# Performance work log

Hardware: AMD Instinct MI355X
Metric: run time of the kernel (lower is better)

## Reference

```python
import math
import jax, jax.numpy as jnp
import numpy as np

B, N, M, C, H, POS = 2, 2048, 64, 256, 8, 6
D = C // H  # head_dim = 32
SCALE = 1.0 / math.sqrt(D)
LAMDA = 1.0


def setup_inputs() -> dict:
    key = jax.random.key(0)
    ks = jax.random.split(key, 15)
    s = 0.05
    return {
        "pairwise_g": jax.random.normal(ks[0], (B, N, N, POS), jnp.float32),
        "coset_functions": jax.random.normal(ks[1], (B, N, C), jnp.float32),
        "mask": jnp.ones((B, N), dtype=bool),
        "Wq": jax.random.normal(ks[2], (C, C), jnp.float32) * s,
        "bq": jax.random.normal(ks[3], (C,), jnp.float32) * s,
        "Wk": jax.random.normal(ks[4], (C, C), jnp.float32) * s,
        "bk": jax.random.normal(ks[5], (C,), jnp.float32) * s,
        "Wl": jax.random.normal(ks[6], (C, POS), jnp.float32) * s,
        "bl": jax.random.normal(ks[7], (C,), jnp.float32) * s,
        "u": jax.random.normal(ks[8], (H, D), jnp.float32) * s,
        "v": jax.random.normal(ks[9], (H, D), jnp.float32) * s,
        "Wi": jax.random.normal(ks[10], (C, C), jnp.float32) * s,
        "bi": jax.random.normal(ks[11], (C,), jnp.float32) * s,
        "Wo": jax.random.normal(ks[12], (C, C), jnp.float32) * s,
        "bo": jax.random.normal(ks[13], (C,), jnp.float32) * s,
    }


def reference(pairwise_g, coset_functions, mask, Wq, bq, Wk, bk, Wl, bl, u, v, Wi, bi, Wo, bo):
    # ---- extract_neighbourhoods (mc_samples=M, fill=1.0 -> k == k_ball, permutation irrelevant)
    dists = jnp.linalg.norm(pairwise_g, axis=-1)                      # (B,N,N)
    dists = jnp.where(mask[:, None, :], dists, jnp.float32(1e8))
    _, nbhd_idx = jax.lax.top_k(-dists, M)                            # (B,N,M) nearest neighbors
    nbhd_pg = jnp.take_along_axis(pairwise_g, nbhd_idx[..., None], axis=2)  # (B,N,M,POS)
    gather_rows = jax.vmap(lambda arr, ix: arr[ix])                   # gather along point axis per batch
    nbhd_cf = gather_rows(coset_functions, nbhd_idx)                  # (B,N,M,C)
    nbhd_mask = gather_rows(mask, nbhd_idx)                           # (B,N,M)

    # ---- RelativePositionKernel
    Q = (coset_functions @ Wq.T + bq).reshape(B, N, H, D).transpose(0, 2, 1, 3)  # (B,H,N,D)
    K = (coset_functions @ Wk.T + bk).reshape(B, N, H, D).transpose(0, 2, 1, 3)  # (B,H,N,D)
    e = (nbhd_pg @ Wl.T + bl).reshape(B, N, M, H, D)                  # (B,N,M,H,D)

    S = jnp.einsum('bhnd,bhkd->bhnk', Q, K)                           # dense scores (as original)
    Sg = jnp.take_along_axis(S, nbhd_idx[:, None, :, :], axis=3)      # (B,H,N,M)
    e_term = jnp.einsum('bnmhd,bhnd->bhnm', e, Q + v[None, :, None, :])
    uK = jnp.einsum('hd,bhkd->bhk', u, K)                             # (B,H,N)
    uKg = jnp.take_along_axis(uK[:, :, None, :], nbhd_idx[:, None, :, :], axis=3)  # (B,H,N,M)
    A = (Sg + LAMDA * e_term + uKg) * SCALE
    A = A.transpose(0, 2, 3, 1)                                       # (B,N,M,H)

    # ---- masked softmax over neighbors
    A = jnp.where(nbhd_mask[..., None], A, jnp.float32(-1e38))
    attn = jax.nn.softmax(A, axis=2)                                  # (B,N,M,H)

    # ---- value projection + weighted sum + output linear
    Vv = (nbhd_cf @ Wi.T + bi).reshape(B, N, M, H, D)                 # (B,N,M,H,D)
    out = jnp.einsum('bnmh,bnmhd->bnhd', attn, Vv).reshape(B, N, C)
    out = out @ Wo.T + bo                                             # (B,N,c_out)
    return out
```

## Files before the change

### kernel.cpp

```cpp
#include <hip/hip_runtime.h>
#include <stdint.h>

#define NB 2
#define NN 2048
#define MM 64
#define CC 256
#define HH 8
#define DD 32
#define PP 6
#define ATT_SCALE 0.17677669529663687f

typedef __attribute__((ext_vector_type(8))) short short8;
typedef __attribute__((ext_vector_type(4))) float f32x4;

__device__ __forceinline__ uint16_t f2bf(float f) {
  union { float f; uint32_t u; } c; c.f = f;
  return (uint16_t)((c.u + 0x7fffu + ((c.u >> 16) & 1u)) >> 16);
}
__device__ __forceinline__ float blo(uint32_t u) {
  union { uint32_t u; float f; } c; c.u = u << 16; return c.f;
}
__device__ __forceinline__ float bhi(uint32_t u) {
  union { uint32_t u; float f; } c; c.u = u & 0xffff0000u; return c.f;
}
__device__ __forceinline__ short8 pack8(float4 a, float4 b) {
  short8 r;
  r[0] = (short)f2bf(a.x); r[1] = (short)f2bf(a.y);
  r[2] = (short)f2bf(a.z); r[3] = (short)f2bf(a.w);
  r[4] = (short)f2bf(b.x); r[5] = (short)f2bf(b.y);
  r[6] = (short)f2bf(b.z); r[7] = (short)f2bf(b.w);
  return r;
}

__global__ __launch_bounds__(64) void k_gemm_qkv(
    const float* __restrict__ A,
    const float* __restrict__ W0, const float* __restrict__ W1, const float* __restrict__ W2,
    const float* __restrict__ b0, const float* __restrict__ b1, const float* __restrict__ b2,
    float* __restrict__ Qo, uint16_t* __restrict__ Ko, uint16_t* __restrict__ Vo) {
  const int z = blockIdx.z;
  const float* W = (z == 0) ? W0 : ((z == 1) ? W1 : W2);
  const float* bias = (z == 0) ? b0 : ((z == 1) ? b1 : b2);

  const int lane = threadIdx.x;
  const int m = lane & 15;
  const int quad = lane >> 4;
  const int row0 = blockIdx.x * 16;
  const int c0 = blockIdx.y * 64;

  f32x4 acc0 = {0.f, 0.f, 0.f, 0.f};
  f32x4 acc1 = {0.f, 0.f, 0.f, 0.f};
  f32x4 acc2 = {0.f, 0.f, 0.f, 0.f};
  f32x4 acc3 = {0.f, 0.f, 0.f, 0.f};

#pragma unroll
  for (int k0 = 0; k0 < CC; k0 += 32) {
    const float4* ap = (const float4*)(A + (size_t)(row0 + m) * CC + k0 + quad * 8);
    const float4* bp0 = (const float4*)(W + (size_t)(c0 + 0 + m) * CC + k0 + quad * 8);
    const float4* bp1 = (const float4*)(W + (size_t)(c0 + 16 + m) * CC + k0 + quad * 8);
    const float4* bp2 = (const float4*)(W + (size_t)(c0 + 32 + m) * CC + k0 + quad * 8);
    const float4* bp3 = (const float4*)(W + (size_t)(c0 + 48 + m) * CC + k0 + quad * 8);
    const short8 a = pack8(ap[0], ap[1]);
    const short8 f0 = pack8(bp0[0], bp0[1]);
    const short8 f1 = pack8(bp1[0], bp1[1]);
    const short8 f2 = pack8(bp2[0], bp2[1]);
    const short8 f3 = pack8(bp3[0], bp3[1]);
    acc0 = __builtin_amdgcn_mfma_f32_16x16x32_bf16(a, f0, acc0, 0, 0, 0);
    acc1 = __builtin_amdgcn_mfma_f32_16x16x32_bf16(a, f1, acc1, 0, 0, 0);
    acc2 = __builtin_amdgcn_mfma_f32_16x16x32_bf16(a, f2, acc2, 0, 0, 0);
    acc3 = __builtin_amdgcn_mfma_f32_16x16x32_bf16(a, f3, acc3, 0, 0, 0);
  }

  const int orow = row0 + quad * 4;
  f32x4 accs[4] = {acc0, acc1, acc2, acc3};
#pragma unroll
  for (int f = 0; f < 4; ++f) {
    const int col = c0 + f * 16 + m;
    const float bv = bias[col];
#pragma unroll
    for (int r = 0; r < 4; ++r) {
      const float val = accs[f][r] + bv;
      const size_t o = (size_t)(orow + r) * CC + col;
      if (z == 0) Qo[o] = val;
      else if (z == 1) Ko[o] = f2bf(val);
      else Vo[o] = f2bf(val);
    }
  }
}

__global__ __launch_bounds__(64) void k_gemm_out(const uint16_t* __restrict__ A,
                                                 const float* __restrict__ W,
                                                 const float* __restrict__ bias,
                                                 float* __restrict__ O) {
  const int lane = threadIdx.x;
  const int m = lane & 15;
  const int quad = lane >> 4;
  const int row0 = blockIdx.x * 16;
  const int c0 = blockIdx.y * 32;

  f32x4 acc0 = {0.f, 0.f, 0.f, 0.f};
  f32x4 acc1 = {0.f, 0.f, 0.f, 0.f};

#pragma unroll
  for (int k0 = 0; k0 < CC; k0 += 32) {
    const short8 a = *(const short8*)(A + (size_t)(row0 + m) * CC + k0 + quad * 8);
    const float4* bp0 = (const float4*)(W + (size_t)(c0 + 0 + m) * CC + k0 + quad * 8);
    const float4* bp1 = (const float4*)(W + (size_t)(c0 + 16 + m) * CC + k0 + quad * 8);
    const short8 f0 = pack8(bp0[0], bp0[1]);
    const short8 f1 = pack8(bp1[0], bp1[1]);
    acc0 = __builtin_amdgcn_mfma_f32_16x16x32_bf16(a, f0, acc0, 0, 0, 0);
    acc1 = __builtin_amdgcn_mfma_f32_16x16x32_bf16(a, f1, acc1, 0, 0, 0);
  }

  const int orow = row0 + quad * 4;
  f32x4 accs[2] = {acc0, acc1};
#pragma unroll
  for (int f = 0; f < 2; ++f) {
    const int col = c0 + f * 16 + m;
    const float bv = bias[col];
#pragma unroll
    for (int r = 0; r < 4; ++r) {
      O[(size_t)(orow + r) * CC + col] = accs[f][r] + bv;
    }
  }
}

__global__ __launch_bounds__(256) void k_fused(const float* __restrict__ pg,
                                               const float* __restrict__ Q,
                                               const uint16_t* __restrict__ K,
                                               const uint16_t* __restrict__ V,
                                               const float* __restrict__ Wl,
                                               const float* __restrict__ bl,
                                               const float* __restrict__ u,
                                               const float* __restrict__ v,
                                               uint16_t* __restrict__ attnV) {
  const int row = blockIdx.x;
  const int b = row >> 11;
  const int t = threadIdx.x;
  const int wave = t >> 6;
  const int lane = t & 63;

  __shared__ float s_mn[4], s_mx[4];
  __shared__ uint32_t s_wsum[4];
  __shared__ uint32_t s_hist[256];
  __shared__ uint32_t s_scan[256];
  __shared__ float s_cd[NN];
  __shared__ int   s_cj[NN];
  __shared__ int s_tbin;
  __shared__ uint32_t s_c0;
  __shared__ int s_cw;
  __shared__ int s_ct;
  __shared__ int s_idx[MM];
  __shared__ float s_npg[MM][7];
  __shared__ float s_qu[CC];
  __shared__ float s_wt[HH][8];
  __shared__ float s_sc[HH][MM];
  __shared__ float s_part[CC];

  const float qv_ = Q[(size_t)row * CC + t];
  s_qu[t] = qv_ + u[t];
  if (t < MM) s_idx[t] = t;

  const float4* base = (const float4*)(pg + (size_t)row * NN * PP);

  float d[8];
  float mn = 3.4e38f, mx = -3.4e38f;
#pragma unroll
  for (int i = 0; i < 4; i++) {
    const int j0 = i * 512 + 2 * t;
    const float4 qa = base[(size_t)(j0 >> 1) * 3 + 0];
    const float4 qb = base[(size_t)(j0 >> 1) * 3 + 1];
    const float4 qc = base[(size_t)(j0 >> 1) * 3 + 2];
    float s0 = __fmul_rn(qa.x, qa.x);
    s0 = __fadd_rn(s0, __fmul_rn(qa.y, qa.y));
    s0 = __fadd_rn(s0, __fmul_rn(qa.z, qa.z));
    s0 = __fadd_rn(s0, __fmul_rn(qa.w, qa.w));
    s0 = __fadd_rn(s0, __fmul_rn(qb.x, qb.x));
    s0 = __fadd_rn(s0, __fmul_rn(qb.y, qb.y));
    float s1 = __fmul_rn(qb.z, qb.z);
    s1 = __fadd_rn(s1, __fmul_rn(qb.w, qb.w));
    s1 = __fadd_rn(s1, __fmul_rn(qc.x, qc.x));
    s1 = __fadd_rn(s1, __fmul_rn(qc.y, qc.y));
    s1 = __fadd_rn(s1, __fmul_rn(qc.z, qc.z));
    s1 = __fadd_rn(s1, __fmul_rn(qc.w, qc.w));
    const float d0 = __fsqrt_rn(s0);
    const float d1 = __fsqrt_rn(s1);
    d[2 * i] = d0; d[2 * i + 1] = d1;
    mn = fminf(mn, fminf(d0, d1));
    mx = fmaxf(mx, fmaxf(d0, d1));
  }

#pragma unroll
  for (int off = 32; off; off >>= 1) {
    mn = fminf(mn, __shfl_xor(mn, off));
    mx = fmaxf(mx, __shfl_xor(mx, off));
  }
  if (lane == 0) { s_mn[wave] = mn; s_mx[wave] = mx; }
  s_hist[t] = 0;
  __syncthreads();
  mn = fminf(fminf(s_mn[0], s_mn[1]), fminf(s_mn[2], s_mn[3]));
  mx = fmaxf(fmaxf(s_mx[0], s_mx[1]), fmaxf(s_mx[2], s_mx[3]));
  const float range = mx - mn;
  const float scale = (range > 0.f) ? (256.0f / range) : 0.f;

  int bins[8];
#pragma unroll
  for (int i = 0; i < 8; i++) {
    int bn = (int)((d[i] - mn) * scale);
    bn = (bn > 255) ? 255 : (bn < 0 ? 0 : bn);
    bins[i] = bn;
    atomicAdd(&s_hist[bn], 1u);
  }
  __syncthreads();

  {
    uint32_t x = s_hist[t];
#pragma unroll
    for (int off = 1; off < 64; off <<= 1) {
      const uint32_t y = __shfl_up(x, off);
      if (lane >= off) x += y;
    }
    if (lane == 63) s_wsum[wave] = x;
    __syncthreads();
    uint32_t pre = 0;
    for (int w = 0; w < wave; w++) pre += s_wsum[w];
    x += pre;
    s_scan[t] = x;
  }
  if (t == 0) { s_cw = 0; s_ct = 0; }
  __syncthreads();

  if (s_scan[t] >= (uint32_t)MM && (t == 0 || s_scan[t - 1] < (uint32_t)MM)) {
    s_tbin = t;
    s_c0 = (t == 0) ? 0u : s_scan[t - 1];
  }
  __syncthreads();

  const int tbin = s_tbin;
  const int c0 = (int)s_c0;

#pragma unroll
  for (int i = 0; i < 8; i++) {
    const int j = (i >> 1) * 512 + 2 * t + (i & 1);
    if (bins[i] < tbin) {
      const int pos = atomicAdd(&s_cw, 1);
      if (pos < MM) s_idx[pos] = j;
    } else if (bins[i] == tbin) {
      const int pos = atomicAdd(&s_ct, 1);
      s_cd[pos] = d[i];
      s_cj[pos] = j;
    }
  }
  __syncthreads();

  if (t < 64) {
    const int cnt = s_ct;
    const int r = MM - c0;
    for (int it = 0; it < r; ++it) {
      float bd = 3.4e38f; int bj = 0x7fffffff; int bi = -1;
      for (int i = t; i < cnt; i += 64) {
        const float dd = s_cd[i]; const int jj = s_cj[i];
        if (dd < bd || (dd == bd && jj < bj)) { bd = dd; bj = jj; bi = i; }
      }
#pragma unroll
      for (int off = 32; off; off >>= 1) {
        const float od = __shfl_xor(bd, off);
        const int oj = __shfl_xor(bj, off);
        const int oi = __shfl_xor(bi, off);
        if (od < bd || (od == bd && oj < bj)) { bd = od; bj = oj; bi = oi; }
      }
      if (t == 0 && bi >= 0) {
        s_cd[bi] = 3.4e38f;
        s_idx[c0 + it] = bj;
      }
      __threadfence_block();
    }
  }
  __syncthreads();

  if (t < MM) {
    const int jj = s_idx[t] & (NN - 1);
    const float2* p = (const float2*)(pg + ((size_t)row * NN + (size_t)jj) * PP);
    const float2 p0 = p[0], p1 = p[1], p2 = p[2];
    s_npg[t][0] = p0.x; s_npg[t][1] = p0.y;
    s_npg[t][2] = p1.x; s_npg[t][3] = p1.y;
    s_npg[t][4] = p2.x; s_npg[t][5] = p2.y;
  }

  {
    const int h = t >> 5;
    const float qpv = qv_ + v[t];
    float part[7];
#pragma unroll
    for (int p = 0; p < 6; p++) part[p] = Wl[(size_t)t * PP + p] * qpv;
    part[6] = bl[t] * qpv;
#pragma unroll
    for (int off = 1; off < 32; off <<= 1) {
#pragma unroll
      for (int p = 0; p < 7; p++) part[p] += __shfl_xor(part[p], off);
    }
    if ((t & 31) == 0) {
#pragma unroll
      for (int p = 0; p < 7; p++) s_wt[h][p] = part[p];
    }
  }
  __syncthreads();

#pragma unroll
  for (int pr = 0; pr < 2; ++pr) {
    const int h = wave + pr * 4;
    const int m = lane;
    const int kidx = s_idx[m] & (NN - 1);
    const uint4* kr = (const uint4*)(K + ((size_t)(b * NN + kidx)) * CC + h * DD);
    float acc = s_wt[h][6];
#pragma unroll
    for (int p = 0; p < 6; p++) acc += s_npg[m][p] * s_wt[h][p];
    const float* qu = &s_qu[h * DD];
    float a2 = 0.f;
#pragma unroll
    for (int w4 = 0; w4 < 4; w4++) {
      const uint4 kv = kr[w4];
      const float* q8 = qu + w4 * 8;
      a2 += q8[0] * blo(kv.x) + q8[1] * bhi(kv.x)
          + q8[2] * blo(kv.y) + q8[3] * bhi(kv.y)
          + q8[4] * blo(kv.z) + q8[5] * bhi(kv.z)
          + q8[6] * blo(kv.w) + q8[7] * bhi(kv.w);
    }
    s_sc[h][m] = (acc + a2) * ATT_SCALE;
  }
  __syncthreads();

#pragma unroll
  for (int pr = 0; pr < 2; ++pr) {
    const int h = wave + pr * 4;
    const float x = s_sc[h][lane];
    float mxv = x;
#pragma unroll
    for (int off = 32; off; off >>= 1) mxv = fmaxf(mxv, __shfl_xor(mxv, off));
    const float e = expf(x - mxv);
    float sm = e;
#pragma unroll
    for (int off = 32; off; off >>= 1) sm += __shfl_xor(sm, off);
    s_sc[h][lane] = e / sm;
  }
  __syncthreads();

  {
    const int h2 = t >> 7;
    const int ci = (t & 127) * 2;
    const int h = ci >> 5;
    const uint32_t* Vb32 = (const uint32_t*)(V + (size_t)b * NN * CC);
    float a0 = 0.f, a1 = 0.f;
#pragma unroll 8
    for (int m = h2; m < MM; m += 2) {
      const uint32_t pv = Vb32[(size_t)(s_idx[m] & (NN - 1)) * (CC / 2) + (ci >> 1)];
      const float p = s_sc[h][m];
      a0 += p * blo(pv);
      a1 += p * bhi(pv);
    }
    if (h2 == 1) { s_part[ci] = a0; s_part[ci + 1] = a1; }
    __syncthreads();
    if (h2 == 0) {
      attnV[(size_t)row * CC + ci]     = f2bf(a0 + s_part[ci]);
      attnV[(size_t)row * CC + ci + 1] = f2bf(a1 + s_part[ci + 1]);
    }
  }
}

extern "C" void kernel_launch(void* const* d_in, const int* in_sizes, int n_in,
                              void* d_out, int out_size, void* d_ws, size_t ws_size,
                              hipStream_t stream) {
  const float* pg = (const float*)d_in[0];
  const float* cf = (const float*)d_in[1];
  const float* Wq = (const float*)d_in[3];
  const float* bq = (const float*)d_in[4];
  const float* Wk = (const float*)d_in[5];
  const float* bk = (const float*)d_in[6];
  const float* Wl = (const float*)d_in[7];
  const float* bl = (const float*)d_in[8];
  const float* u  = (const float*)d_in[9];
  const float* v  = (const float*)d_in[10];
  const float* Wi = (const float*)d_in[11];
  const float* bi = (const float*)d_in[12];
  const float* Wo = (const float*)d_in[13];
  const float* bo = (const float*)d_in[14];

  char* ws = (char*)d_ws;
  float* Q  = (float*)ws;
  uint16_t* K = (uint16_t*)(ws + (size_t)4 * (1 << 20));
  uint16_t* V = (uint16_t*)(ws + (size_t)6 * (1 << 20));
  uint16_t* aV = (uint16_t*)(ws + (size_t)8 * (1 << 20));
  float* out = (float*)d_out;

  hipLaunchKernelGGL(k_gemm_qkv, dim3(256, 4, 3), dim3(64), 0, stream,
                     cf, Wq, Wk, Wi, bq, bk, bi, Q, K, V);
  hipLaunchKernelGGL(k_fused, dim3(NB * NN), dim3(256), 0, stream,
                     pg, Q, K, V, Wl, bl, u, v, aV);
  hipLaunchKernelGGL(k_gemm_out, dim3(256, 8), dim3(64), 0, stream,
                     aV, Wo, bo, out);
}
```

Before: 358.0 us.

## Overlap QKV GEMM with neighbour selection in one launch and pre-convert to bf16

Adds a prep kernel that converts the features and all weight matrices to bf16 once. The QKV GEMM is merged into the neighbour-selection kernel as extra blocks, so the GEMM and the distance/top-k selection, which does not depend on Q/K/V, run concurrently. The attention part is split into its own kernel that reads the selected indices and gathered positions from workspace. This removes the serialisation between the GEMM and the bandwidth-bound selection, and the repeated float-to-bf16 packing inside the GEMMs. In exchange it adds an extra launch and a workspace round trip for idx and npg, and the selection blocks now have less shared memory and a smaller s_cj array.

```diff
diff --git a/kernel.cpp b/kernel.cpp
--- a/kernel.cpp
+++ b/kernel.cpp
@@ -9,6 +9,7 @@
 #define DD 32
 #define PP 6
 #define ATT_SCALE 0.17677669529663687f
+#define NGEMMB 768
 
 typedef __attribute__((ext_vector_type(8))) short short8;
 typedef __attribute__((ext_vector_type(4))) float f32x4;
@@ -23,141 +24,104 @@
 __device__ __forceinline__ float bhi(uint32_t u) {
   union { uint32_t u; float f; } c; c.u = u & 0xffff0000u; return c.f;
 }
-__device__ __forceinline__ short8 pack8(float4 a, float4 b) {
-  short8 r;
-  r[0] = (short)f2bf(a.x); r[1] = (short)f2bf(a.y);
-  r[2] = (short)f2bf(a.z); r[3] = (short)f2bf(a.w);
-  r[4] = (short)f2bf(b.x); r[5] = (short)f2bf(b.y);
-  r[6] = (short)f2bf(b.z); r[7] = (short)f2bf(b.w);
-  return r;
-}
-
-__global__ __launch_bounds__(64) void k_gemm_qkv(
-    const float* __restrict__ A,
-    const float* __restrict__ W0, const float* __restrict__ W1, const float* __restrict__ W2,
-    const float* __restrict__ b0, const float* __restrict__ b1, const float* __restrict__ b2,
-    float* __restrict__ Qo, uint16_t* __restrict__ Ko, uint16_t* __restrict__ Vo) {
-  const int z = blockIdx.z;
-  const float* W = (z == 0) ? W0 : ((z == 1) ? W1 : W2);
-  const float* bias = (z == 0) ? b0 : ((z == 1) ? b1 : b2);
-
-  const int lane = threadIdx.x;
-  const int m = lane & 15;
-  const int quad = lane >> 4;
-  const int row0 = blockIdx.x * 16;
-  const int c0 = blockIdx.y * 64;
-
-  f32x4 acc0 = {0.f, 0.f, 0.f, 0.f};
-  f32x4 acc1 = {0.f, 0.f, 0.f, 0.f};
-  f32x4 acc2 = {0.f, 0.f, 0.f, 0.f};
-  f32x4 acc3 = {0.f, 0.f, 0.f, 0.f};
-
-#pragma unroll
-  for (int k0 = 0; k0 < CC; k0 += 32) {
-    const float4* ap = (const float4*)(A + (size_t)(row0 + m) * CC + k0 + quad * 8);
-    const float4* bp0 = (const float4*)(W + (size_t)(c0 + 0 + m) * CC + k0 + quad * 8);
-    const float4* bp1 = (const float4*)(W + (size_t)(c0 + 16 + m) * CC + k0 + quad * 8);
-    const float4* bp2 = (const float4*)(W + (size_t)(c0 + 32 + m) * CC + k0 + quad * 8);
-    const float4* bp3 = (const float4*)(W + (size_t)(c0 + 48 + m) * CC + k0 + quad * 8);
-    const short8 a = pack8(ap[0], ap[1]);
-    const short8 f0 = pack8(bp0[0], bp0[1]);
-    const short8 f1 = pack8(bp1[0], bp1[1]);
-    const short8 f2 = pack8(bp2[0], bp2[1]);
-    const short8 f3 = pack8(bp3[0], bp3[1]);
-    acc0 = __builtin_amdgcn_mfma_f32_16x16x32_bf16(a, f0, acc0, 0, 0, 0);
-    acc1 = __builtin_amdgcn_mfma_f32_16x16x32_bf16(a, f1, acc1, 0, 0, 0);
-    acc2 = __builtin_amdgcn_mfma_f32_16x16x32_bf16(a, f2, acc2, 0, 0, 0);
-    acc3 = __builtin_amdgcn_mfma_f32_16x16x32_bf16(a, f3, acc3, 0, 0, 0);
-  }
-
-  const int orow = row0 + quad * 4;
-  f32x4 accs[4] = {acc0, acc1, acc2, acc3};
-#pragma unroll
-  for (int f = 0; f < 4; ++f) {
-    const int col = c0 + f * 16 + m;
-    const float bv = bias[col];
-#pragma unroll
-    for (int r = 0; r < 4; ++r) {
-      const float val = accs[f][r] + bv;
-      const size_t o = (size_t)(orow + r) * CC + col;
-      if (z == 0) Qo[o] = val;
-      else if (z == 1) Ko[o] = f2bf(val);
-      else Vo[o] = f2bf(val);
-    }
-  }
-}
-
-__global__ __launch_bounds__(64) void k_gemm_out(const uint16_t* __restrict__ A,
-                                                 const float* __restrict__ W,
-                                                 const float* __restrict__ bias,
-                                                 float* __restrict__ O) {
-  const int lane = threadIdx.x;
-  const int m = lane & 15;
-  const int quad = lane >> 4;
-  const int row0 = blockIdx.x * 16;
-  const int c0 = blockIdx.y * 32;
-
-  f32x4 acc0 = {0.f, 0.f, 0.f, 0.f};
-  f32x4 acc1 = {0.f, 0.f, 0.f, 0.f};
-
-#pragma unroll
-  for (int k0 = 0; k0 < CC; k0 += 32) {
-    const short8 a = *(const short8*)(A + (size_t)(row0 + m) * CC + k0 + quad * 8);
-    const float4* bp0 = (const float4*)(W + (size_t)(c0 + 0 + m) * CC + k0 + quad * 8);
-    const float4* bp1 = (const float4*)(W + (size_t)(c0 + 16 + m) * CC + k0 + quad * 8);
-    const short8 f0 = pack8(bp0[0], bp0[1]);
-    const short8 f1 = pack8(bp1[0], bp1[1]);
-    acc0 = __builtin_amdgcn_mfma_f32_16x16x32_bf16(a, f0, acc0, 0, 0, 0);
-    acc1 = __builtin_amdgcn_mfma_f32_16x16x32_bf16(a, f1, acc1, 0, 0, 0);
-  }
-
-  const int orow = row0 + quad * 4;
-  f32x4 accs[2] = {acc0, acc1};
-#pragma unroll
-  for (int f = 0; f < 2; ++f) {
-    const int col = c0 + f * 16 + m;
-    const float bv = bias[col];
-#pragma unroll
-    for (int r = 0; r < 4; ++r) {
-      O[(size_t)(orow + r) * CC + col] = accs[f][r] + bv;
-    }
-  }
-}
-
-__global__ __launch_bounds__(256) void k_fused(const float* __restrict__ pg,
-                                               const float* __restrict__ Q,
-                                               const uint16_t* __restrict__ K,
-                                               const uint16_t* __restrict__ V,
-                                               const float* __restrict__ Wl,
-                                               const float* __restrict__ bl,
-                                               const float* __restrict__ u,
-                                               const float* __restrict__ v,
-                                               uint16_t* __restrict__ attnV) {
-  const int row = blockIdx.x;
-  const int b = row >> 11;
-  const int t = threadIdx.x;
-  const int wave = t >> 6;
-  const int lane = t & 63;
-
+
+__global__ __launch_bounds__(256) void k_prep(
+    const float* __restrict__ cf,
+    const float* __restrict__ Wq, const float* __restrict__ Wk,
+    const float* __restrict__ Wi, const float* __restrict__ Wo,
+    uint16_t* __restrict__ cfb, uint16_t* __restrict__ Wb) {
+  const int tid = blockIdx.x * 256 + threadIdx.x;
+  const int e0 = tid * 4;
+  const int CFN = NB * NN * CC;
+  const float* src;
+  uint16_t* dst;
+  if (e0 < CFN) {
+    src = cf + e0; dst = cfb + e0;
+  } else {
+    const int w = e0 - CFN;
+    const int which = w >> 16;
+    const int off = w & 65535;
+    if (which == 0) src = Wq + off;
+    else if (which == 1) src = Wk + off;
+    else if (which == 2) src = Wi + off;
+    else src = Wo + off;
+    dst = Wb + w;
+  }
+  const float4 x = *(const float4*)src;
+  ushort4 o;
+  o.x = f2bf(x.x); o.y = f2bf(x.y); o.z = f2bf(x.z); o.w = f2bf(x.w);
+  *(ushort4*)dst = o;
+}
+
+__global__ __launch_bounds__(256) void k_select_qkv(
+    const float* __restrict__ pg,
+    const uint16_t* __restrict__ cfb, const uint16_t* __restrict__ Wb,
+    const float* __restrict__ bq, const float* __restrict__ bk, const float* __restrict__ bi,
+    float* __restrict__ Qo, uint16_t* __restrict__ Ko, uint16_t* __restrict__ Vo,
+    int* __restrict__ idx_out, float* __restrict__ npg_out) {
   __shared__ float s_mn[4], s_mx[4];
   __shared__ uint32_t s_wsum[4];
   __shared__ uint32_t s_hist[256];
   __shared__ uint32_t s_scan[256];
   __shared__ float s_cd[NN];
-  __shared__ int   s_cj[NN];
+  __shared__ uint16_t s_cj[NN];
   __shared__ int s_tbin;
   __shared__ uint32_t s_c0;
   __shared__ int s_cw;
   __shared__ int s_ct;
   __shared__ int s_idx[MM];
-  __shared__ float s_npg[MM][7];
-  __shared__ float s_qu[CC];
-  __shared__ float s_wt[HH][8];
-  __shared__ float s_sc[HH][MM];
-  __shared__ float s_part[CC];
-
-  const float qv_ = Q[(size_t)row * CC + t];
-  s_qu[t] = qv_ + u[t];
+
+  if (blockIdx.x < NGEMMB) {
+    const int task = blockIdx.x * 4 + (threadIdx.x >> 6);
+    const int z = task >> 10;
+    const int rem = task & 1023;
+    const int row0 = (rem & 255) * 16;
+    const int c0 = (rem >> 8) * 64;
+    const uint16_t* W = Wb + (size_t)z * (CC * CC);
+    const float* bias = (z == 0) ? bq : ((z == 1) ? bk : bi);
+    const int lane = threadIdx.x & 63;
+    const int m = lane & 15;
+    const int quad = lane >> 4;
+
+    f32x4 acc0 = {0.f, 0.f, 0.f, 0.f};
+    f32x4 acc1 = {0.f, 0.f, 0.f, 0.f};
+    f32x4 acc2 = {0.f, 0.f, 0.f, 0.f};
+    f32x4 acc3 = {0.f, 0.f, 0.f, 0.f};
+#pragma unroll
+    for (int k0 = 0; k0 < CC; k0 += 32) {
+      const short8 a  = *(const short8*)(cfb + (size_t)(row0 + m) * CC + k0 + quad * 8);
+      const short8 f0 = *(const short8*)(W + (size_t)(c0 + 0 + m) * CC + k0 + quad * 8);
+      const short8 f1 = *(const short8*)(W + (size_t)(c0 + 16 + m) * CC + k0 + quad * 8);
+      const short8 f2 = *(const short8*)(W + (size_t)(c0 + 32 + m) * CC + k0 + quad * 8);
+      const short8 f3 = *(const short8*)(W + (size_t)(c0 + 48 + m) * CC + k0 + quad * 8);
+      acc0 = __builtin_amdgcn_mfma_f32_16x16x32_bf16(a, f0, acc0, 0, 0, 0);
+      acc1 = __builtin_amdgcn_mfma_f32_16x16x32_bf16(a, f1, acc1, 0, 0, 0);
+      acc2 = __builtin_amdgcn_mfma_f32_16x16x32_bf16(a, f2, acc2, 0, 0, 0);
+      acc3 = __builtin_amdgcn_mfma_f32_16x16x32_bf16(a, f3, acc3, 0, 0, 0);
+    }
+    const int orow = row0 + quad * 4;
+    f32x4 accs[4] = {acc0, acc1, acc2, acc3};
+#pragma unroll
+    for (int f = 0; f < 4; ++f) {
+      const int col = c0 + f * 16 + m;
+      const float bv = bias[col];
+#pragma unroll
+      for (int r = 0; r < 4; ++r) {
+        const float val = accs[f][r] + bv;
+        const size_t o = (size_t)(orow + r) * CC + col;
+        if (z == 0) Qo[o] = val;
+        else if (z == 1) Ko[o] = f2bf(val);
+        else Vo[o] = f2bf(val);
+      }
+    }
+    return;
+  }
+
+  const int row = blockIdx.x - NGEMMB;
+  const int t = threadIdx.x;
+  const int wave = t >> 6;
+  const int lane = t & 63;
+
   if (t < MM) s_idx[t] = t;
 
   const float4* base = (const float4*)(pg + (size_t)row * NN * PP);
@@ -247,7 +211,7 @@
     } else if (bins[i] == tbin) {
       const int pos = atomicAdd(&s_ct, 1);
       s_cd[pos] = d[i];
-      s_cj[pos] = j;
+      s_cj[pos] = (uint16_t)j;
     }
   }
   __syncthreads();
@@ -256,20 +220,20 @@
     const int cnt = s_ct;
     const int r = MM - c0;
     for (int it = 0; it < r; ++it) {
-      float bd = 3.4e38f; int bj = 0x7fffffff; int bi = -1;
+      float bd = 3.4e38f; int bj = 0x7fffffff; int bi_ = -1;
       for (int i = t; i < cnt; i += 64) {
-        const float dd = s_cd[i]; const int jj = s_cj[i];
-        if (dd < bd || (dd == bd && jj < bj)) { bd = dd; bj = jj; bi = i; }
+        const float dd = s_cd[i]; const int jj = (int)s_cj[i];
+        if (dd < bd || (dd == bd && jj < bj)) { bd = dd; bj = jj; bi_ = i; }
       }
 #pragma unroll
       for (int off = 32; off; off >>= 1) {
         const float od = __shfl_xor(bd, off);
         const int oj = __shfl_xor(bj, off);
-        const int oi = __shfl_xor(bi, off);
-        if (od < bd || (od == bd && oj < bj)) { bd = od; bj = oj; bi = oi; }
+        const int oi = __shfl_xor(bi_, off);
+        if (od < bd || (od == bd && oj < bj)) { bd = od; bj = oj; bi_ = oi; }
       }
-      if (t == 0 && bi >= 0) {
-        s_cd[bi] = 3.4e38f;
+      if (t == 0 && bi_ >= 0) {
+        s_cd[bi_] = 3.4e38f;
         s_idx[c0 + it] = bj;
       }
       __threadfence_block();
@@ -279,8 +243,40 @@
 
   if (t < MM) {
     const int jj = s_idx[t] & (NN - 1);
+    idx_out[(size_t)row * MM + t] = jj;
     const float2* p = (const float2*)(pg + ((size_t)row * NN + (size_t)jj) * PP);
     const float2 p0 = p[0], p1 = p[1], p2 = p[2];
+    float2* np = (float2*)(npg_out + ((size_t)row * MM + t) * PP);
+    np[0] = p0; np[1] = p1; np[2] = p2;
+  }
+}
+
+__global__ __launch_bounds__(256) void k_attn(
+    const float* __restrict__ Q, const uint16_t* __restrict__ K,
+    const uint16_t* __restrict__ V,
+    const float* __restrict__ Wl, const float* __restrict__ bl,
+    const float* __restrict__ u, const float* __restrict__ v,
+    const int* __restrict__ idx_in, const float* __restrict__ npg_in,
+    uint16_t* __restrict__ attnV) {
+  const int row = blockIdx.x;
+  const int b = row >> 11;
+  const int t = threadIdx.x;
+  const int wave = t >> 6;
+  const int lane = t & 63;
+
+  __shared__ int s_idx[MM];
+  __shared__ float s_npg[MM][7];
+  __shared__ float s_qu[CC];
+  __shared__ float s_wt[HH][8];
+  __shared__ float s_sc[HH][MM];
+  __shared__ float s_part[CC];
+
+  const float qv_ = Q[(size_t)row * CC + t];
+  s_qu[t] = qv_ + u[t];
+  if (t < MM) {
+    s_idx[t] = idx_in[(size_t)row * MM + t];
+    const float2* np = (const float2*)(npg_in + ((size_t)row * MM + t) * PP);
+    const float2 p0 = np[0], p1 = np[1], p2 = np[2];
     s_npg[t][0] = p0.x; s_npg[t][1] = p0.y;
     s_npg[t][2] = p1.x; s_npg[t][3] = p1.y;
     s_npg[t][4] = p2.x; s_npg[t][5] = p2.y;
@@ -362,6 +358,41 @@
     if (h2 == 0) {
       attnV[(size_t)row * CC + ci]     = f2bf(a0 + s_part[ci]);
       attnV[(size_t)row * CC + ci + 1] = f2bf(a1 + s_part[ci + 1]);
+    }
+  }
+}
+
+__global__ __launch_bounds__(64) void k_gemm_out(const uint16_t* __restrict__ A,
+                                                 const uint16_t* __restrict__ W,
+                                                 const float* __restrict__ bias,
+                                                 float* __restrict__ O) {
+  const int lane = threadIdx.x;
+  const int m = lane & 15;
+  const int quad = lane >> 4;
+  const int row0 = blockIdx.x * 16;
+  const int c0 = blockIdx.y * 32;
+
+  f32x4 acc0 = {0.f, 0.f, 0.f, 0.f};
+  f32x4 acc1 = {0.f, 0.f, 0.f, 0.f};
+
+#pragma unroll
+  for (int k0 = 0; k0 < CC; k0 += 32) {
+    const short8 a  = *(const short8*)(A + (size_t)(row0 + m) * CC + k0 + quad * 8);
+    const short8 f0 = *(const short8*)(W + (size_t)(c0 + 0 + m) * CC + k0 + quad * 8);
+    const short8 f1 = *(const short8*)(W + (size_t)(c0 + 16 + m) * CC + k0 + quad * 8);
+    acc0 = __builtin_amdgcn_mfma_f32_16x16x32_bf16(a, f0, acc0, 0, 0, 0);
+    acc1 = __builtin_amdgcn_mfma_f32_16x16x32_bf16(a, f1, acc1, 0, 0, 0);
+  }
+
+  const int orow = row0 + quad * 4;
+  f32x4 accs[2] = {acc0, acc1};
+#pragma unroll
+  for (int f = 0; f < 2; ++f) {
+    const int col = c0 + f * 16 + m;
+    const float bv = bias[col];
+#pragma unroll
+    for (int r = 0; r < 4; ++r) {
+      O[(size_t)(orow + r) * CC + col] = accs[f][r] + bv;
     }
   }
 }
@@ -385,16 +416,22 @@
   const float* bo = (const float*)d_in[14];
 
   char* ws = (char*)d_ws;
-  float* Q  = (float*)ws;
-  uint16_t* K = (uint16_t*)(ws + (size_t)4 * (1 << 20));
-  uint16_t* V = (uint16_t*)(ws + (size_t)6 * (1 << 20));
-  uint16_t* aV = (uint16_t*)(ws + (size_t)8 * (1 << 20));
+  float* Q      = (float*)ws;
+  uint16_t* K   = (uint16_t*)(ws + (size_t)4  * (1 << 20));
+  uint16_t* V   = (uint16_t*)(ws + (size_t)6  * (1 << 20));
+  uint16_t* aV  = (uint16_t*)(ws + (size_t)8  * (1 << 20));
+  uint16_t* cfb = (uint16_t*)(ws + (size_t)10 * (1 << 20));
+  uint16_t* Wb  = (uint16_t*)(ws + (size_t)12 * (1 << 20));
+  int* idxb     = (int*)(ws + (size_t)12 * (1 << 20) + (512 << 10));
+  float* npgb   = (float*)(ws + (size_t)13 * (1 << 20) + (512 << 10));
   float* out = (float*)d_out;
 
-  hipLaunchKernelGGL(k_gemm_qkv, dim3(256, 4, 3), dim3(64), 0, stream,
-                     cf, Wq, Wk, Wi, bq, bk, bi, Q, K, V);
-  hipLaunchKernelGGL(k_fused, dim3(NB * NN), dim3(256), 0, stream,
-                     pg, Q, K, V, Wl, bl, u, v, aV);
+  hipLaunchKernelGGL(k_prep, dim3(1280), dim3(256), 0, stream,
+                     cf, Wq, Wk, Wi, Wo, cfb, Wb);
+  hipLaunchKernelGGL(k_select_qkv, dim3(NGEMMB + NB * NN), dim3(256), 0, stream,
+                     pg, cfb, Wb, bq, bk, bi, Q, K, V, idxb, npgb);
+  hipLaunchKernelGGL(k_attn, dim3(NB * NN), dim3(256), 0, stream,
+                     Q, K, V, Wl, bl, u, v, idxb, npgb, aV);
   hipLaunchKernelGGL(k_gemm_out, dim3(256, 8), dim3(64), 0, stream,
-                     aV, Wo, bo, out);
-}
+                     aV, Wb + (size_t)3 * CC * CC, bo, out);
+}
```

After: 356.7 us. No clear change (-0.4%).
